# Kernel optimization log

Measured on AMD Instinct MI355X. Metric: run time of the kernel, lower is better.

## Reference

```python
import jax, jax.numpy as jnp
import numpy as np

B, D, L, H = 4, 1024, 2048, 8
HD = D // H


def setup_inputs() -> dict:
    key = jax.random.key(0)
    k1, k2, k3, k4 = jax.random.split(key, 4)
    query = jax.random.normal(k1, (B, D, L), dtype=jnp.float32)
    mask = jax.random.randint(k2, (B, L), 0, 2, dtype=jnp.int32)
    W1 = jax.random.normal(k3, (2 * D, D), dtype=jnp.float32) * (D ** -0.5)
    Wq = jax.random.normal(k4, (D, D), dtype=jnp.float32) * (D ** -0.5)
    return {"query": query, "mask": mask, "W1": W1, "Wq": Wq}


def _split_heads(x):
    # [B, L, C] -> [B, H, L, C//H]
    b, l, c = x.shape
    return x.reshape(b, l, H, c // H).transpose(0, 2, 1, 3)


def reference(query, mask, W1, Wq):
    # 1x1 conv == channel GEMM; produce [B, L, out]
    temp = jnp.einsum('od,bdl->blo', W1, query)   # [B, L, 2D] (K|V)
    q = jnp.einsum('od,bdl->blo', Wq, query)      # [B, L, D]
    k, v = jnp.split(temp, 2, axis=-1)
    q = _split_heads(q) * (HD ** -0.5)            # [B, H, L, HD]
    k = _split_heads(k)
    v = _split_heads(v)
    scores = jnp.einsum('bhqd,bhkd->bhqk', q, k)  # [B, H, L, L]
    m = mask.astype(jnp.float32)[:, None, None, :]
    logits = scores + (-1e30) * (1.0 - m)
    weights = jax.nn.softmax(logits, axis=-1)     # dropout p=0 (eval)
    out = jnp.einsum('bhqk,bhkd->bhqd', weights, v)
    out = out.transpose(0, 2, 1, 3).reshape(B, L, D)  # merge heads
    return out.transpose(0, 2, 1)                 # [B, D, L]
```

## Files before the change

### kernel.cpp

```cpp
#include <hip/hip_runtime.h>
#include <hip/hip_bf16.h>

#define B_  4
#define D_  1024
#define L_  2048
#define H_  8
#define HD_ 128

typedef __attribute__((ext_vector_type(8))) short bf16x8;
typedef __attribute__((ext_vector_type(4))) float f32x4;
typedef __attribute__((ext_vector_type(2))) unsigned uint2v;
typedef __attribute__((ext_vector_type(4))) unsigned uint4v;

#if __has_builtin(__builtin_amdgcn_permlane16_swap) && __has_builtin(__builtin_amdgcn_permlane32_swap)
#define HAS_PERMSWAP 1
#else
#define HAS_PERMSWAP 0
#endif

static __device__ __forceinline__ ushort f2bf(float f) {
    unsigned u = __float_as_uint(f);
    unsigned r = (u + 0x7fffu + ((u >> 16) & 1u)) >> 16;
    return (ushort)r;
}

static __device__ __forceinline__ unsigned cvt_pk_bf16(float lo, float hi) {
    unsigned r;
    asm("v_cvt_pk_bf16_f32 %0, %1, %2" : "=v"(r) : "v"(lo), "v"(hi));
    return r;
}

static __device__ __forceinline__ float exp2_fast(float x) {
#if __has_builtin(__builtin_amdgcn_exp2f)
    return __builtin_amdgcn_exp2f(x);
#else
    return exp2f(x);
#endif
}

static __device__ __forceinline__ float qmax4(float x) {
#if HAS_PERMSWAP
    uint2v a = __builtin_amdgcn_permlane16_swap(__float_as_uint(x), __float_as_uint(x), false, false);
    float y = fmaxf(__uint_as_float(a[0]), __uint_as_float(a[1]));
    uint2v b = __builtin_amdgcn_permlane32_swap(__float_as_uint(y), __float_as_uint(y), false, false);
    return fmaxf(__uint_as_float(b[0]), __uint_as_float(b[1]));
#else
    x = fmaxf(x, __shfl_xor(x, 16, 64));
    return fmaxf(x, __shfl_xor(x, 32, 64));
#endif
}

static __device__ __forceinline__ void dma16(const ushort* g, ushort* l) {
    __builtin_amdgcn_global_load_lds(
        (const __attribute__((address_space(1))) void*)g,
        (__attribute__((address_space(3))) void*)l, 16, 0, 0);
}

__global__ void k_zero_out(float* __restrict__ out, int n) {
    int i = blockIdx.x * 256 + threadIdx.x;
    if (i < n) out[i] = 0.f;
}

__global__ void k_prep(const float* __restrict__ q, const float* __restrict__ W1,
                       const float* __restrict__ Wq, const int* __restrict__ mask,
                       ushort* __restrict__ Wb, ushort* __restrict__ Xt,
                       int* __restrict__ cidx, int* __restrict__ cnt) {
    __shared__ float tile[32][33];
    const int bid = blockIdx.x, t = threadIdx.x;
    if (bid < 8192) {
        int bx = bid & 63, by = (bid >> 6) & 31, bz = bid >> 11;
        int tx = t & 31, ty = t >> 5;
        int d0 = by * 32, l0 = bx * 32;
        const float* src = q + (size_t)bz * D_ * L_;
        for (int i = 0; i < 4; i++)
            tile[ty + 8 * i][tx] = src[(size_t)(d0 + ty + 8 * i) * L_ + l0 + tx];
        __syncthreads();
        ushort* dst = Xt + (size_t)bz * L_ * D_;
        for (int i = 0; i < 4; i++)
            dst[(size_t)(l0 + ty + 8 * i) * D_ + d0 + tx] = f2bf(tile[tx][ty + 8 * i]);
    } else if (bid < 8192 + 3072) {
        int i = (bid - 8192) * 256 + t;
        const int n1 = 2 * D_ * D_ / 4;
        float4 v = (i < n1) ? ((const float4*)W1)[i] : ((const float4*)Wq)[i - n1];
        ushort4 o;
        o.x = f2bf(v.x); o.y = f2bf(v.y); o.z = f2bf(v.z); o.w = f2bf(v.w);
        ((ushort4*)Wb)[i] = o;
    } else {
        int b = bid - (8192 + 3072);
        if (t < 64) {
            int lane = t;
            const int* mb = mask + b * L_;
            int base = 0;
            for (int c = 0; c < L_; c += 64) {
                int m = mb[c + lane];
                unsigned long long bal = __ballot(m != 0);
                int pre = __popcll(bal & ((1ull << lane) - 1ull));
                if (m) cidx[b * L_ + base + pre] = c + lane;
                base += __popcll(bal);
            }
            for (int j = base + lane; j < L_; j += 64) cidx[b * L_ + j] = 0;
            if (lane == 0) cnt[b] = base;
        }
    }
}

__launch_bounds__(256)
__global__ void k_proj(const ushort* __restrict__ Wb, const ushort* __restrict__ Xt,
                       const int* __restrict__ cidx, const int* __restrict__ cnt,
                       ushort* __restrict__ Qb, ushort* __restrict__ Kb,
                       ushort* __restrict__ Vt) {
    __shared__ alignas(16) ushort As[128 * 64];
    __shared__ alignas(16) ushort Bs[128 * 64];
    const int b  = blockIdx.z;
    const int o0 = blockIdx.y * 128;
    const int l0 = blockIdx.x * 128;
    const int type = o0 >> 10;
    if (type < 2) {
        int tiles = (cnt[b] + 127) >> 7;
        if (blockIdx.x >= tiles) return;
    }
    const int t = threadIdx.x;
    const int wave = t >> 6, lane = t & 63, quad = lane >> 4, li = lane & 15;
    const int wm = wave >> 1, wn = wave & 1;
    const ushort* Xb = Xt + (size_t)b * L_ * D_;

    const int srow = t >> 3;
    const int g = (t & 7) ^ (srow & 7);
    const ushort* aSrc[4];
    const ushort* bSrc[4];
    for (int i = 0; i < 4; i++) {
        int r = i * 32 + srow;
        aSrc[i] = Wb + (size_t)(o0 + r) * D_ + g * 8;
        int l = l0 + r;
        int gl = (type < 2) ? cidx[b * L_ + l] : l;
        bSrc[i] = Xb + (size_t)gl * D_ + g * 8;
    }

    f32x4 acc[4][4] = {};

    for (int k0 = 0; k0 < D_; k0 += 64) {
        for (int i = 0; i < 4; i++)
            dma16(aSrc[i] + k0, &As[(i * 256 + wave * 64) * 8]);
        for (int i = 0; i < 4; i++)
            dma16(bSrc[i] + k0, &Bs[(i * 256 + wave * 64) * 8]);
        __syncthreads();
        for (int ks = 0; ks < 64; ks += 32) {
            const int kc = ks >> 3;
            bf16x8 af[4], bfr[4];
            for (int mf = 0; mf < 4; mf++) {
                int row = wm * 64 + mf * 16 + li;
                af[mf] = *(const bf16x8*)&As[row * 64 + (((kc + quad) ^ (li & 7)) * 8)];
            }
            for (int nf = 0; nf < 4; nf++) {
                int row = wn * 64 + nf * 16 + li;
                bfr[nf] = *(const bf16x8*)&Bs[row * 64 + (((kc + quad) ^ (li & 7)) * 8)];
            }
            for (int mf = 0; mf < 4; mf++)
                for (int nf = 0; nf < 4; nf++)
                    acc[mf][nf] = __builtin_amdgcn_mfma_f32_16x16x32_bf16(af[mf], bfr[nf], acc[mf][nf], 0, 0, 0);
        }
        __syncthreads();
    }

    const float qscale = 0.1275174495450826f;
    for (int mf = 0; mf < 4; mf++) {
        int o = o0 + wm * 64 + mf * 16 + quad * 4;
        int c = o & 1023;
        int h = c >> 7, hd = c & 127;
        for (int nf = 0; nf < 4; nf++) {
            int l = l0 + wn * 64 + nf * 16 + li;
            f32x4 v = acc[mf][nf];
            if (type == 0) {
                uint2 kk;
                kk.x = cvt_pk_bf16(v[0], v[1]);
                kk.y = cvt_pk_bf16(v[2], v[3]);
                *(uint2*)&Kb[(((size_t)(b * H_ + h)) * L_ + l) * HD_ + hd] = kk;
            } else if (type == 1) {
                size_t base = (size_t)(b * H_ + h) * HD_;
                Vt[(base + hd + 0) * L_ + l] = f2bf(v[0]);
                Vt[(base + hd + 1) * L_ + l] = f2bf(v[1]);
                Vt[(base + hd + 2) * L_ + l] = f2bf(v[2]);
                Vt[(base + hd + 3) * L_ + l] = f2bf(v[3]);
            } else {
                uint2 qq;
                qq.x = cvt_pk_bf16(v[0] * qscale, v[1] * qscale);
                qq.y = cvt_pk_bf16(v[2] * qscale, v[3] * qscale);
                *(uint2*)&Qb[(((size_t)(b * H_ + h)) * L_ + l) * HD_ + hd] = qq;
            }
        }
    }
}

__launch_bounds__(256, 4)
__global__ void k_attn(const ushort* __restrict__ Qb, const ushort* __restrict__ Kb,
                       const ushort* __restrict__ Vt, const int* __restrict__ mask,
                       float* __restrict__ out) {
    __shared__ alignas(16) ushort Ks[2][32][128];
    __shared__ alignas(16) ushort Vs[2][128][32];
#if !HAS_PERMSWAP
    __shared__ alignas(16) ushort Pl[4][16][40];
#endif
    const int blk = blockIdx.x;
    const int h = blk & 7, qt = (blk >> 3) & 31, b = blk >> 8;
    const int t = threadIdx.x;
    const int w = t >> 6, lane = t & 63, quad = lane >> 4, li = lane & 15;
    const int q0 = qt * 64 + w * 16;
    const ushort* Qh = Qb + (size_t)(b * H_ + h) * L_ * HD_;
    const ushort* Kh = Kb + (size_t)(b * H_ + h) * L_ * HD_;
    const ushort* Vh = Vt + (size_t)(b * H_ + h) * HD_ * L_;
    const int* mb = mask + b * L_;

    int cm = 0;
    for (int c = lane; c < L_; c += 64) cm += mb[c];
    cm += __shfl_xor(cm, 32, 64);
    cm += __shfl_xor(cm, 16, 64);
    cm += __shfl_xor(cm, 8, 64);
    cm += __shfl_xor(cm, 4, 64);
    cm += __shfl_xor(cm, 2, 64);
    cm += __shfl_xor(cm, 1, 64);
    const int cnt = cm;
    int cnt_pad = (cnt + 31) & ~31;
    if (cnt_pad < 32) cnt_pad = 32;

    const ushort* kgp[2]; const ushort* vgp[2];
    for (int i = 0; i < 2; i++) {
        int seg = w * 2 + i;
        int key = seg * 4 + (lane >> 4);
        int ck  = (lane & 15) ^ (key & 15);
        kgp[i] = Kh + (size_t)key * HD_ + ck * 8;
        int hd  = seg * 16 + (lane >> 2);
        int cv  = (lane & 3) ^ (hd & 3);
        vgp[i] = Vh + (size_t)hd * L_ + cv * 8;
    }

    for (int i = 0; i < 2; i++) dma16(kgp[i], &Ks[0][0][0] + (w * 2 + i) * 512);
    for (int i = 0; i < 2; i++) dma16(vgp[i], &Vs[0][0][0] + (w * 2 + i) * 512);

    bf16x8 qf[4];
    for (int kf = 0; kf < 4; kf++)
        qf[kf] = *(const bf16x8*)&Qh[(size_t)(q0 + li) * HD_ + kf * 32 + quad * 8];

    bf16x8 ones;
    for (int i = 0; i < 8; i++) ones[i] = (short)0x3F80;

    float mrun = -1e30f;
    f32x4 lsum = {};
    f32x4 acc[8] = {};

    int buf = 0;
    for (int n0 = 0; n0 < cnt_pad; n0 += 32, buf ^= 1) {
        __syncthreads();

        if (n0 + 32 < cnt_pad) {
            int nb = buf ^ 1;
            for (int i = 0; i < 2; i++)
                dma16(kgp[i] + (size_t)(n0 + 32) * HD_, &Ks[nb][0][0] + (w * 2 + i) * 512);
            for (int i = 0; i < 2; i++)
                dma16(vgp[i] + (n0 + 32), &Vs[nb][0][0] + (w * 2 + i) * 512);
        }

        f32x4 s[2] = {};
        for (int kf = 0; kf < 4; kf++) {
            bf16x8 kfr[2];
            for (int mt = 0; mt < 2; mt++)
                kfr[mt] = *(const bf16x8*)&Ks[buf][mt * 16 + li][((kf * 4 + quad) ^ li) * 8];
            for (int mt = 0; mt < 2; mt++)
                s[mt] = __builtin_amdgcn_mfma_f32_16x16x32_bf16(kfr[mt], qf[kf], s[mt], 0, 0, 0);
        }

        if (n0 + 32 > cnt) {
            for (int mt = 0; mt < 2; mt++)
                for (int r = 0; r < 4; r++)
                    if (n0 + mt * 16 + quad * 4 + r >= cnt) s[mt][r] = -1e30f;
        }

        float a0 = fmaxf(fmaxf(s[0][0], s[0][1]), fmaxf(s[0][2], s[0][3]));
        float a1 = fmaxf(fmaxf(s[1][0], s[1][1]), fmaxf(s[1][2], s[1][3]));
        float nm = qmax4(fmaxf(a0, a1));
        float mnew = fmaxf(mrun, nm);
        float alpha = exp2_fast(mrun - mnew);
        mrun = mnew;
        for (int mt = 0; mt < 2; mt++)
            for (int r = 0; r < 4; r++)
                s[mt][r] = exp2_fast(s[mt][r] - mnew);

        if (__any(alpha != 1.0f)) {
            int sb = (lane & 48) | (quad * 4);
            float ar0 = __shfl(alpha, sb + 0, 64);
            float ar1 = __shfl(alpha, sb + 1, 64);
            float ar2 = __shfl(alpha, sb + 2, 64);
            float ar3 = __shfl(alpha, sb + 3, 64);
            lsum[0] *= ar0; lsum[1] *= ar1; lsum[2] *= ar2; lsum[3] *= ar3;
            for (int nf2 = 0; nf2 < 8; nf2++) {
                acc[nf2][0] *= ar0;
                acc[nf2][1] *= ar1;
                acc[nf2][2] *= ar2;
                acc[nf2][3] *= ar3;
            }
        }

        bf16x8 pa;
#if HAS_PERMSWAP
        {
            unsigned c0 = cvt_pk_bf16(s[0][0], s[0][1]);
            unsigned c1 = cvt_pk_bf16(s[0][2], s[0][3]);
            unsigned c2 = cvt_pk_bf16(s[1][0], s[1][1]);
            unsigned c3 = cvt_pk_bf16(s[1][2], s[1][3]);
            uint2v x02 = __builtin_amdgcn_permlane32_swap(c0, c2, false, false);
            uint2v u02 = __builtin_amdgcn_permlane16_swap(x02[0], x02[1], false, false);
            uint2v x13 = __builtin_amdgcn_permlane32_swap(c1, c3, false, false);
            uint2v u13 = __builtin_amdgcn_permlane16_swap(x13[0], x13[1], false, false);
            uint4v paw;
            paw[0] = u02[0];
            paw[1] = u13[0];
            paw[2] = u02[1];
            paw[3] = u13[1];
            pa = __builtin_bit_cast(bf16x8, paw);
        }
#else
        {
            for (int mt = 0; mt < 2; mt++) {
                uint2 pk;
                pk.x = cvt_pk_bf16(s[mt][0], s[mt][1]);
                pk.y = cvt_pk_bf16(s[mt][2], s[mt][3]);
                *(uint2*)&Pl[w][li][mt * 16 + quad * 4] = pk;
            }
            pa = *(const bf16x8*)&Pl[w][li][quad * 8];
        }
#endif

        lsum = __builtin_amdgcn_mfma_f32_16x16x32_bf16(pa, ones, lsum, 0, 0, 0);

        for (int nf2 = 0; nf2 < 8; nf2++) {
            bf16x8 vb = *(const bf16x8*)&Vs[buf][nf2 * 16 + li][(quad ^ (li & 3)) * 8];
            acc[nf2] = __builtin_amdgcn_mfma_f32_16x16x32_bf16(pa, vb, acc[nf2], 0, 0, 0);
        }
    }

    float i0 = 1.0f / lsum[0];
    float i1 = 1.0f / lsum[1];
    float i2 = 1.0f / lsum[2];
    float i3 = 1.0f / lsum[3];
    int l = q0 + quad * 4;
    for (int nf2 = 0; nf2 < 8; nf2++) {
        int d = h * HD_ + nf2 * 16 + li;
        float4 o4 = { acc[nf2][0] * i0, acc[nf2][1] * i1,
                      acc[nf2][2] * i2, acc[nf2][3] * i3 };
        *(float4*)&out[((size_t)(b * D_ + d)) * L_ + l] = o4;
    }
}

extern "C" void kernel_launch(void* const* d_in, const int* in_sizes, int n_in,
                              void* d_out, int out_size, void* d_ws, size_t ws_size,
                              hipStream_t stream) {
    const float* query = nullptr;
    const int*   mask  = nullptr;
    const float* W1    = nullptr;
    const float* Wq    = nullptr;
    for (int i = 0; i < n_in; i++) {
        switch (in_sizes[i]) {
            case 8388608: query = (const float*)d_in[i]; break;
            case 8192:    mask  = (const int*)d_in[i];   break;
            case 2097152: W1    = (const float*)d_in[i]; break;
            case 1048576: Wq    = (const float*)d_in[i]; break;
        }
    }
    float* out = (float*)d_out;

    if (ws_size < 50331648u || !query || !mask || !W1 || !Wq) {
        hipLaunchKernelGGL(k_zero_out, dim3((out_size + 255) / 256), dim3(256), 0, stream,
                           out, out_size);
        return;
    }

    ushort* Wb = (ushort*)d_out;
    ushort* Xt = (ushort*)((char*)d_out + 6291456);
    int* cidx  = (int*)((char*)d_out + 23068672);
    int* cnt   = (int*)((char*)d_out + 23101440);
    char* ws = (char*)d_ws;
    ushort* Qb = (ushort*)(ws + 0);
    ushort* Kb = (ushort*)(ws + 16777216);
    ushort* Vt = (ushort*)(ws + 33554432);

    hipLaunchKernelGGL(k_prep, dim3(8192 + 3072 + 4), dim3(256), 0, stream,
                       query, W1, Wq, mask, Wb, Xt, cidx, cnt);
    hipLaunchKernelGGL(k_proj, dim3(16, 24, 4), dim3(256), 0, stream, Wb, Xt, cidx, cnt, Qb, Kb, Vt);
    hipLaunchKernelGGL(k_attn, dim3(1024), dim3(256), 0, stream, Qb, Kb, Vt, mask, out);
}
```

Baseline: 224.7 us.

## Double-buffer projection GEMM, remap blocks per XCD, widen transpose tiles

The projection GEMM now uses two LDS buffers. The global-to-LDS DMA for the next K slice is issued while the current slice feeds the MFMAs, which removes one barrier per iteration. Blocks are launched on a 1D grid and remapped so that consecutive work ids on each XCD cover 4x4 groups of tiles, meant to improve L2 reuse. The prep transpose switches to 64x64 tiles with float4 loads and packed bf16 stores. Together these double the projection kernel's LDS use, which may lower occupancy.

```diff
diff --git a/kernel.cpp b/kernel.cpp
--- a/kernel.cpp
+++ b/kernel.cpp
@@ -65,28 +65,10 @@
                        const float* __restrict__ Wq, const int* __restrict__ mask,
                        ushort* __restrict__ Wb, ushort* __restrict__ Xt,
                        int* __restrict__ cidx, int* __restrict__ cnt) {
-    __shared__ float tile[32][33];
+    __shared__ float tile[64][65];
     const int bid = blockIdx.x, t = threadIdx.x;
-    if (bid < 8192) {
-        int bx = bid & 63, by = (bid >> 6) & 31, bz = bid >> 11;
-        int tx = t & 31, ty = t >> 5;
-        int d0 = by * 32, l0 = bx * 32;
-        const float* src = q + (size_t)bz * D_ * L_;
-        for (int i = 0; i < 4; i++)
-            tile[ty + 8 * i][tx] = src[(size_t)(d0 + ty + 8 * i) * L_ + l0 + tx];
-        __syncthreads();
-        ushort* dst = Xt + (size_t)bz * L_ * D_;
-        for (int i = 0; i < 4; i++)
-            dst[(size_t)(l0 + ty + 8 * i) * D_ + d0 + tx] = f2bf(tile[tx][ty + 8 * i]);
-    } else if (bid < 8192 + 3072) {
-        int i = (bid - 8192) * 256 + t;
-        const int n1 = 2 * D_ * D_ / 4;
-        float4 v = (i < n1) ? ((const float4*)W1)[i] : ((const float4*)Wq)[i - n1];
-        ushort4 o;
-        o.x = f2bf(v.x); o.y = f2bf(v.y); o.z = f2bf(v.z); o.w = f2bf(v.w);
-        ((ushort4*)Wb)[i] = o;
-    } else {
-        int b = bid - (8192 + 3072);
+    if (bid < 4) {
+        int b = bid;
         if (t < 64) {
             int lane = t;
             const int* mb = mask + b * L_;
@@ -101,6 +83,36 @@
             for (int j = base + lane; j < L_; j += 64) cidx[b * L_ + j] = 0;
             if (lane == 0) cnt[b] = base;
         }
+    } else if (bid < 4 + 2048) {
+        int tb = bid - 4;
+        int bx = tb & 31, by = (tb >> 5) & 15, bz = tb >> 9;
+        int l0 = bx * 64, d0 = by * 64;
+        int rr = t >> 4, cc = t & 15;
+        const float* src = q + (size_t)bz * D_ * L_;
+        for (int i = 0; i < 4; i++) {
+            int r = rr + 16 * i;
+            float4 v = *(const float4*)&src[(size_t)(d0 + r) * L_ + l0 + cc * 4];
+            tile[r][cc * 4 + 0] = v.x;
+            tile[r][cc * 4 + 1] = v.y;
+            tile[r][cc * 4 + 2] = v.z;
+            tile[r][cc * 4 + 3] = v.w;
+        }
+        __syncthreads();
+        ushort* dst = Xt + (size_t)bz * L_ * D_;
+        for (int i = 0; i < 4; i++) {
+            int lr = rr + 16 * i;
+            uint2 o;
+            o.x = cvt_pk_bf16(tile[cc * 4 + 0][lr], tile[cc * 4 + 1][lr]);
+            o.y = cvt_pk_bf16(tile[cc * 4 + 2][lr], tile[cc * 4 + 3][lr]);
+            *(uint2*)&dst[(size_t)(l0 + lr) * D_ + d0 + cc * 4] = o;
+        }
+    } else {
+        int i = (bid - 2052) * 256 + t;
+        const int n1 = 2 * D_ * D_ / 4;
+        float4 v = (i < n1) ? ((const float4*)W1)[i] : ((const float4*)Wq)[i - n1];
+        ushort4 o;
+        o.x = f2bf(v.x); o.y = f2bf(v.y); o.z = f2bf(v.z); o.w = f2bf(v.w);
+        ((ushort4*)Wb)[i] = o;
     }
 }
 
@@ -109,15 +121,23 @@
                        const int* __restrict__ cidx, const int* __restrict__ cnt,
                        ushort* __restrict__ Qb, ushort* __restrict__ Kb,
                        ushort* __restrict__ Vt) {
-    __shared__ alignas(16) ushort As[128 * 64];
-    __shared__ alignas(16) ushort Bs[128 * 64];
-    const int b  = blockIdx.z;
-    const int o0 = blockIdx.y * 128;
-    const int l0 = blockIdx.x * 128;
+    __shared__ alignas(16) ushort As[2][128 * 64];
+    __shared__ alignas(16) ushort Bs[2][128 * 64];
+    const int bid = blockIdx.x;
+    const int xcd = bid & 7, j = bid >> 3;
+    const int wid = xcd * 192 + j;
+    const int st = wid >> 4, m = wid & 15;
+    const int b  = st / 24;
+    const int sr = st % 24;
+    const int sx = sr & 3, sy = sr >> 2;
+    const int x  = sx * 4 + (m & 3);
+    const int y  = sy * 4 + (m >> 2);
+    const int o0 = y * 128;
+    const int l0 = x * 128;
     const int type = o0 >> 10;
     if (type < 2) {
         int tiles = (cnt[b] + 127) >> 7;
-        if (blockIdx.x >= tiles) return;
+        if (x >= tiles) return;
     }
     const int t = threadIdx.x;
     const int wave = t >> 6, lane = t & 63, quad = lane >> 4, li = lane & 15;
@@ -138,28 +158,36 @@
 
     f32x4 acc[4][4] = {};
 
-    for (int k0 = 0; k0 < D_; k0 += 64) {
-        for (int i = 0; i < 4; i++)
-            dma16(aSrc[i] + k0, &As[(i * 256 + wave * 64) * 8]);
-        for (int i = 0; i < 4; i++)
-            dma16(bSrc[i] + k0, &Bs[(i * 256 + wave * 64) * 8]);
+    for (int i = 0; i < 4; i++) dma16(aSrc[i], &As[0][(i * 256 + wave * 64) * 8]);
+    for (int i = 0; i < 4; i++) dma16(bSrc[i], &Bs[0][(i * 256 + wave * 64) * 8]);
+
+    int buf = 0;
+    for (int k0 = 0; k0 < D_; k0 += 64, buf ^= 1) {
         __syncthreads();
+
+        if (k0 + 64 < D_) {
+            int nb = buf ^ 1;
+            for (int i = 0; i < 4; i++)
+                dma16(aSrc[i] + k0 + 64, &As[nb][(i * 256 + wave * 64) * 8]);
+            for (int i = 0; i < 4; i++)
+                dma16(bSrc[i] + k0 + 64, &Bs[nb][(i * 256 + wave * 64) * 8]);
+        }
+
         for (int ks = 0; ks < 64; ks += 32) {
             const int kc = ks >> 3;
             bf16x8 af[4], bfr[4];
             for (int mf = 0; mf < 4; mf++) {
                 int row = wm * 64 + mf * 16 + li;
-                af[mf] = *(const bf16x8*)&As[row * 64 + (((kc + quad) ^ (li & 7)) * 8)];
+                af[mf] = *(const bf16x8*)&As[buf][row * 64 + (((kc + quad) ^ (li & 7)) * 8)];
             }
             for (int nf = 0; nf < 4; nf++) {
                 int row = wn * 64 + nf * 16 + li;
-                bfr[nf] = *(const bf16x8*)&Bs[row * 64 + (((kc + quad) ^ (li & 7)) * 8)];
+                bfr[nf] = *(const bf16x8*)&Bs[buf][row * 64 + (((kc + quad) ^ (li & 7)) * 8)];
             }
             for (int mf = 0; mf < 4; mf++)
                 for (int nf = 0; nf < 4; nf++)
                     acc[mf][nf] = __builtin_amdgcn_mfma_f32_16x16x32_bf16(af[mf], bfr[nf], acc[mf][nf], 0, 0, 0);
         }
-        __syncthreads();
     }
 
     const float qscale = 0.1275174495450826f;
@@ -382,8 +410,8 @@
     ushort* Kb = (ushort*)(ws + 16777216);
     ushort* Vt = (ushort*)(ws + 33554432);
 
-    hipLaunchKernelGGL(k_prep, dim3(8192 + 3072 + 4), dim3(256), 0, stream,
+    hipLaunchKernelGGL(k_prep, dim3(4 + 2048 + 3072), dim3(256), 0, stream,
                        query, W1, Wq, mask, Wb, Xt, cidx, cnt);
-    hipLaunchKernelGGL(k_proj, dim3(16, 24, 4), dim3(256), 0, stream, Wb, Xt, cidx, cnt, Qb, Kb, Vt);
+    hipLaunchKernelGGL(k_proj, dim3(1536), dim3(256), 0, stream, Wb, Xt, cidx, cnt, Qb, Kb, Vt);
     hipLaunchKernelGGL(k_attn, dim3(1024), dim3(256), 0, stream, Qb, Kb, Vt, mask, out);
 }
```

After: 218.1 us. -2.9%, faster.
